# Kernel optimization log

Measured on AMD Instinct MI355X. Metric: run time of the kernel, lower is better.

Reference implementation:

```python
import jax, jax.numpy as jnp
import numpy as np
from jax import lax

V, E, H, B, P, Q = 50000, 300, 256, 32, 400, 40


def _cell(x, h, c, Wih, Whh, b):
    # torch nn.LSTMCell math (b = b_ih + b_hh), gate order i,f,g,o
    g = x @ Wih.T + h @ Whh.T + b
    i, f, gg, o = jnp.split(g, 4, axis=-1)
    c2 = jax.nn.sigmoid(f) * c + jax.nn.sigmoid(i) * jnp.tanh(gg)
    return jax.nn.sigmoid(o) * jnp.tanh(c2), c2


def setup_inputs():
    key = jax.random.key(0)
    ks = jax.random.split(key, 26)
    n = lambda k, s: jax.random.normal(k, s, jnp.float32) * 0.05
    return {
        "passage_ids": jax.random.randint(ks[0], (P, B), 0, V),
        "question_ids": jax.random.randint(ks[1], (Q, B), 0, V),
        "passage_lens": jax.random.randint(ks[2], (B,), P // 2, P + 1),
        "question_lens": jax.random.randint(ks[3], (B,), Q // 2, Q + 1),
        "answer": jax.random.randint(ks[4], (2, B), 0, P // 2),
        "embed": n(ks[5], (V, E)),
        "pre_Wih": n(ks[6], (4 * H, E)),
        "pre_Whh": n(ks[7], (4 * H, H)),
        "pre_b": n(ks[8], (4 * H,)),
        "Wq": n(ks[9], (H, H)),
        "Wp": n(ks[10], (H, H)),
        "bp": n(ks[11], (H,)),
        "Wh": n(ks[12], (H, H)),
        "w_alpha": n(ks[13], (H,)),
        "b_alpha": n(ks[14], ()),
        "m_Wih": n(ks[15], (4 * H, 2 * H)),
        "m_Whh": n(ks[16], (4 * H, H)),
        "m_b": n(ks[17], (4 * H,)),
        "Wm": n(ks[18], (2 * H, H)),
        "Wa": n(ks[19], (H, H)),
        "ba": n(ks[20], (H,)),
        "w_beta": n(ks[21], (H,)),
        "b_beta": n(ks[22], ()),
        "p_Wih": n(ks[23], (4 * H, 2 * H)),
        "p_Whh": n(ks[24], (4 * H, H)),
        "p_b": n(ks[25], (4 * H,)),
    }


def _forward(embed, pre_Wih, pre_Whh, pre_b, Wq, Wp, bp, Wh, w_alpha, b_alpha,
             m_Wih, m_Whh, m_b, Wm, Wa, ba, w_beta, b_beta, p_Wih, p_Whh, p_b,
             passage_ids, passage_lens, question_ids, question_lens):
    Hd = pre_Whh.shape[1]
    Bd = passage_ids.shape[1]
    z0 = jnp.zeros((Bd, Hd), jnp.float32)

    def preprocess(ids, lens):
        x = embed[ids]                                       # [T,B,E]
        T = x.shape[0]
        m = (jnp.arange(T)[:, None] < lens[None, :]).astype(jnp.float32)[:, :, None]  # [T,B,1]
        def step(carry, inp):
            h, c = carry
            xt, mt = inp
            _, c2 = _cell(xt, h, c, pre_Wih, pre_Whh, pre_b)
            h2 = jnp.tanh(c2) * mt                           # module quirk: h := tanh(c)
            return (h2, c2 * mt), h2
        _, Hs = lax.scan(step, (z0, z0), (x, m))
        return Hs, m

    Hp, mP = preprocess(passage_ids, passage_lens)           # [P,B,H]
    Hq, _ = preprocess(question_ids, question_lens)          # [Q,B,H]

    attQ = Hq @ Wq                                           # [Q,B,H]

    def match(Hp_dir, m_dir):
        def step(carry, inp):
            h, c = carry
            hp, mt = inp                                     # hp [B,H], mt [B,1]
            g = jnp.tanh(attQ + hp @ Wp + bp + h @ Wh)       # [Q,B,H]
            alpha = jax.nn.softmax(g @ w_alpha + b_alpha, axis=0)  # softmax over question time [Q,B]
            wq = jnp.einsum('qb,qbh->bh', alpha, Hq)
            zt = jnp.concatenate([hp, wq], axis=-1) * mt
            h2, c2 = _cell(zt, h, c, m_Wih, m_Whh, m_b)
            h2 = h2 * mt
            return (h2, c2 * mt), h2
        _, Hs = lax.scan(step, (z0, z0), (Hp_dir, m_dir))
        return Hs

    Hf = match(Hp, mP)
    Hb = match(Hp[::-1], mP[::-1])[::-1]
    Hr = jnp.concatenate([Hf, Hb], axis=-1)                  # [P,B,2H]

    attM = Hr @ Wm                                           # [P,B,H]
    valid = (jnp.arange(Hr.shape[0])[:, None] < passage_lens[None, :]).astype(jnp.float32)  # [P,B]
    ha, ca = z0, z0
    dists = []
    for _ in range(2):                                       # start / end pointer
        Fk = jnp.tanh(attM + ha @ Wa + ba)                   # [P,B,H]
        scores = Fk @ w_beta + b_beta                        # [P,B]
        scores = jnp.where(valid > 0, scores, -1e30)
        beta = jax.nn.softmax(scores, axis=0) * valid        # zeros past passage length, like original
        dists.append(beta.T)                                 # [B,P]
        wHr = jnp.einsum('pb,pbh->bh', beta, Hr)
        ha, ca = _cell(wHr, ha, ca, p_Wih, p_Whh, p_b)
    return jnp.stack(dists)                                  # [2,B,P]


def reference(passage_ids, question_ids, passage_lens, question_lens, answer,
              embed, pre_Wih, pre_Whh, pre_b, Wq, Wp, bp, Wh, w_alpha, b_alpha,
              m_Wih, m_Whh, m_b, Wm, Wa, ba, w_beta, b_beta, p_Wih, p_Whh, p_b):
    # `answer` only feeds the training loss in the original; forward returns the distributions.
    return _forward(embed, pre_Wih, pre_Whh, pre_b, Wq, Wp, bp, Wh, w_alpha, b_alpha,
                    m_Wih, m_Whh, m_b, Wm, Wa, ba, w_beta, b_beta, p_Wih, p_Whh, p_b,
                    passage_ids, passage_lens, question_ids, question_lens)
```

## Files before the change

### kernel.cpp

```cpp
#include <hip/hip_runtime.h>
#include <hip/hip_bf16.h>

typedef __attribute__((ext_vector_type(8))) short short8;
typedef __attribute__((ext_vector_type(4))) float f32x4;
typedef __attribute__((ext_vector_type(2))) float f32x2;
typedef unsigned short u16;
typedef unsigned int u32;

#define DEV __device__ __forceinline__

static constexpr int Hd    = 256;
static constexpr int Bb    = 32;
static constexpr int Pp    = 400;
static constexpr int Qq    = 40;
static constexpr int NROWS = Pp * Bb + Qq * Bb;
static constexpr int PROBE_MAGIC = 1234567;

DEV float bf2f(u16 u) { u32 i = ((u32)u) << 16; float f; __builtin_memcpy(&f, &i, 4); return f; }
DEV u16 f2bf(float f) { u32 i; __builtin_memcpy(&i, &f, 4); i += 0x7FFFu + ((i >> 16) & 1u); return (u16)(i >> 16); }
DEV float sigf(float x) { return __builtin_amdgcn_rcpf(1.f + __expf(-x)); }
DEV float tanhf_(float x) {
  float ax = __builtin_fabsf(x);
  float t = __expf(2.f * ax);
  float r = 1.f - 2.f * __builtin_amdgcn_rcpf(t + 1.f);
  return x < 0.f ? -r : r;
}
DEV f32x4 mfma32(short8 a, short8 b, f32x4 c) {
  return __builtin_amdgcn_mfma_f32_16x16x32_bf16(a, b, c, 0, 0, 0);
}
DEV short8 zero8() { short8 z = {0,0,0,0,0,0,0,0}; return z; }

struct KArgs {
  const int *pids, *qids, *plen, *qlen;
  const float *embedF, *preWihF, *preWhhF, *preBF, *WqF, *WpF, *bpF, *WhF,
              *walphaF, *balphaF, *mWihF, *mWhhF, *mBF, *WmF, *WaF, *baF,
              *wbetaF, *bbetaF, *pWihF, *pWhhF, *pBF;
  int* bar;
  u16 *WqT, *WpT, *WmT, *WihP, *Xpad, *preX, *Hp, *Hq, *Hrb, *wq, *wHr, *haB,
      *attQb, *pWihB, *pWhhB;
  float *hpWp, *attM, *pe, *scores, *aWa, *gatesW;
  float* out;
};

DEV void probe_mark(int* bar, int idx) {
  if (blockIdx.x == 0 && threadIdx.x == 0)
    __hip_atomic_store(bar + 768 + idx, PROBE_MAGIC, __ATOMIC_RELEASE, __HIP_MEMORY_SCOPE_AGENT);
}

DEV void barn(int* base, int grp, int n, int gen) {
  __syncthreads();
  if (threadIdx.x == 0) {
    int* c = base + grp * 128;
    int* g = base + grp * 128 + 64;
    if (__hip_atomic_fetch_add(c, 1, __ATOMIC_ACQ_REL, __HIP_MEMORY_SCOPE_AGENT) == n - 1) {
      __hip_atomic_store(c, 0, __ATOMIC_RELAXED, __HIP_MEMORY_SCOPE_AGENT);
      __hip_atomic_store(g, gen, __ATOMIC_RELEASE, __HIP_MEMORY_SCOPE_AGENT);
    } else {
      while (__hip_atomic_load(g, __ATOMIC_ACQUIRE, __HIP_MEMORY_SCOPE_AGENT) < gen) {}
    }
  }
  __syncthreads();
}

__global__ __launch_bounds__(256) void k_prep(KArgs A) {
  const int gtid = blockIdx.x * 256 + threadIdx.x;
  const int GS = 256 * 256;
  for (int idx = gtid; idx < 1024 * 160; idx += GS) {
    int row = idx / 160, cd = idx - row * 160;
    u32 v = 0;
    if (cd < 150) {
      f32x2 e2 = *(const f32x2*)(A.preWihF + (size_t)row * 300 + cd * 2);
      v = (u32)f2bf(e2[0]) | ((u32)f2bf(e2[1]) << 16);
    }
    *(u32*)(A.WihP + (size_t)row * 320 + cd * 2) = v;
  }
  for (int idx = gtid; idx < NROWS * 160; idx += GS) {
    int row = idx / 160, cd = idx - row * 160;
    int id = (row < Pp * Bb) ? A.pids[row] : A.qids[row - Pp * Bb];
    u32 v = 0;
    if (cd < 150) {
      f32x2 e2 = *(const f32x2*)(A.embedF + (size_t)id * 300 + cd * 2);
      v = (u32)f2bf(e2[0]) | ((u32)f2bf(e2[1]) << 16);
    }
    *(u32*)(A.Xpad + (size_t)row * 320 + cd * 2) = v;
  }
  for (int idx = gtid; idx < 65536; idx += GS) {
    int r = idx >> 8, c = idx & 255;
    A.WqT[idx] = f2bf(A.WqF[c * 256 + r]);
    A.WpT[idx] = f2bf(A.WpF[c * 256 + r]);
  }
  for (int idx = gtid; idx < 131072; idx += GS) {
    int r = idx >> 9, c = idx & 511;
    A.WmT[idx] = f2bf(A.WmF[c * 256 + r]);
  }
  for (int idx = gtid; idx < 524288 + 262144; idx += GS) {
    if (idx < 524288) A.pWihB[idx] = f2bf(A.pWihF[idx]);
    else              A.pWhhB[idx - 524288] = f2bf(A.pWhhF[idx - 524288]);
  }
  if (gtid < 32 * 256) {
    A.aWa[gtid] = A.baF[gtid & 255];
    A.haB[gtid] = 0;
  }
  probe_mark(A.bar, 0);
}

struct GemmArgs { const u16* Ag; int lda; const u16* Bg; int ldb; int Mt64, Nt64, nk; float* Cf; u16* Cb; int ldc; int* bar; int probe; };

__global__ __launch_bounds__(512) void k_gemm(GemmArgs g) {
  const int tid = threadIdx.x, lane = tid & 63;
  const int r16 = lane & 15, kl = (lane >> 4) * 8;
  const int ntile = g.Mt64 * g.Nt64;
  const int stride = gridDim.x * 8;
  for (int tix = blockIdx.x * 8 + (tid >> 6); tix < ntile; tix += stride) {
    int m0 = (tix / g.Nt64) * 64, n0 = (tix % g.Nt64) * 64;
    f32x4 acc[4][4] = {};
    for (int kb = 0; kb < g.nk; ++kb) {
      int k0 = kb * 32 + kl;
      short8 a[4], b[4];
#pragma unroll
      for (int i = 0; i < 4; ++i) {
        a[i] = *(const short8*)(g.Ag + (size_t)(m0 + i * 16 + r16) * g.lda + k0);
        b[i] = *(const short8*)(g.Bg + (size_t)(n0 + i * 16 + r16) * g.ldb + k0);
      }
#pragma unroll
      for (int mi = 0; mi < 4; ++mi)
#pragma unroll
        for (int ni = 0; ni < 4; ++ni) acc[mi][ni] = mfma32(a[mi], b[ni], acc[mi][ni]);
    }
#pragma unroll
    for (int mi = 0; mi < 4; ++mi)
#pragma unroll
      for (int ni = 0; ni < 4; ++ni)
#pragma unroll
        for (int j = 0; j < 4; ++j) {
          int r = m0 + mi * 16 + (lane >> 4) * 4 + j, cc = n0 + ni * 16 + r16;
          if (g.Cf) g.Cf[(size_t)r * g.ldc + cc] = acc[mi][ni][j];
          else      g.Cb[(size_t)r * g.ldc + cc] = f2bf(acc[mi][ni][j]);
        }
  }
  probe_mark(g.bar, g.probe);
}

__global__ __launch_bounds__(512) void k_prescan(KArgs A) {
  __shared__ __align__(16) unsigned char sm[33280];
  float* PRE = (float*)(sm + 24576);
  float* CL  = (float*)(sm + 30720);
  float* PBL = (float*)(sm + 32768);
  const int blk = blockIdx.x;
  const int gi  = blk & 15;
  const int grp = blk >> 4;
  const int steps  = grp ? Qq : Pp;
  const int* lens  = grp ? A.qlen : A.plen;
  u16* Hs          = grp ? A.Hq : A.Hp;
  const int xoff   = grp ? Pp * Bb : 0;

  const int tid = threadIdx.x, lane = tid & 63, wv = tid >> 6;
  const int r16 = lane & 15, kl = (lane >> 4) * 8;
  const int h0 = gi * 16;

  for (int idx = tid; idx < 48 * 256; idx += 512) {
    int row = idx >> 8, k = idx & 255;
    int gate = (row >> 4) * 256 + h0 + (row & 15);
    int byte = row * 512 + ((2 * k) ^ ((row & 7) << 4));
    *(u16*)(sm + byte) = f2bf(A.preWhhF[(size_t)gate * 256 + k]);
  }
  for (int idx = tid; idx < 32 * 16; idx += 512) CL[idx] = 0.f;
  if (tid < 48) PBL[tid] = A.preBF[(tid >> 4) * 256 + h0 + (tid & 15)];
  __syncthreads();

  int gen = 0;
#pragma unroll 1
  for (int t = 0; t < steps; ++t) {
    if (wv < 6) {
      int mi = wv & 1, ni = wv >> 1;
      int chain = mi * 16 + r16;
      f32x4 acc = {0.f, 0.f, 0.f, 0.f};
#pragma unroll
      for (int kb = 0; kb < 8; ++kb) {
        int k0 = kb * 32 + kl;
        short8 a = zero8();
        if (t > 0) a = *(const short8*)(Hs + (size_t)((t - 1) * 32 + chain) * 256 + k0);
        int row = ni * 16 + r16;
        short8 b = *(const short8*)(sm + row * 512 + ((2 * k0) ^ ((row & 7) << 4)));
        acc = mfma32(a, b, acc);
      }
      int col = ni * 16 + r16;
#pragma unroll
      for (int j = 0; j < 4; ++j)
        PRE[(mi * 16 + (lane >> 4) * 4 + j) * 48 + col] = acc[j];
    }
    __syncthreads();
    {
      int chain = tid >> 4, hd = tid & 15;
      size_t xr = (size_t)(xoff + t * 32 + chain) * 1024;
      float ip = PRE[chain * 48 + hd]      + bf2f(A.preX[xr + h0 + hd])       + PBL[hd];
      float fp = PRE[chain * 48 + 16 + hd] + bf2f(A.preX[xr + 256 + h0 + hd]) + PBL[16 + hd];
      float gp = PRE[chain * 48 + 32 + hd] + bf2f(A.preX[xr + 512 + h0 + hd]) + PBL[32 + hd];
      float c2 = sigf(fp) * CL[chain * 16 + hd] + sigf(ip) * tanhf_(gp);
      float mt = (t < lens[chain]) ? 1.f : 0.f;
      float h2 = tanhf_(c2) * mt;
      c2 *= mt;
      CL[chain * 16 + hd] = c2;
      Hs[(size_t)(t * 32 + chain) * 256 + h0 + hd] = f2bf(h2);
    }
    barn(A.bar, grp, 16, ++gen);
  }
  probe_mark(A.bar, 2);
}

__global__ __launch_bounds__(512) void k_match(KArgs A) {
  __shared__ __align__(16) unsigned char sm[122880];
  u16*   WHT = (u16*)(sm + 98304);
  float* PRE = (float*)(sm + 106496);
  float* CL  = (float*)(sm + 114688);
  float* EL  = (float*)(sm + 116736);
  u16*   H2L = (u16*)(sm + 118784);
  float* SL  = (float*)(sm + 119808);
  float* AL  = (float*)(sm + 120128);
  float* BPL = (float*)(sm + 120448);
  float* WAL = (float*)(sm + 121472);
  float* MBL = (float*)(sm + 122496);

  const int blk = blockIdx.x;
  const int gi  = blk & 15;
  const int dir = blk >> 4;
  const int grp = 2 + dir;
  const int tid = threadIdx.x, lane = tid & 63, wv = tid >> 6;
  const int r16 = lane & 15, kl = (lane >> 4) * 8;
  const int h0 = gi * 16;
  float* peBlk = A.pe + (size_t)((dir * 16 + gi) * 32) * 256;

  for (int idx = tid; idx < 64 * 768; idx += 512) {
    int row = idx / 768, k = idx - row * 768;
    int gate = (row >> 4) * 256 + h0 + (row & 15);
    float v = (k < 512) ? A.mWihF[(size_t)gate * 512 + k] : A.mWhhF[(size_t)gate * 256 + (k - 512)];
    int byte = row * 1536 + ((2 * k) ^ ((row & 7) << 4));
    *(u16*)(sm + byte) = f2bf(v);
  }
  for (int idx = tid; idx < 256 * 16; idx += 512) {
    int h = idx >> 4, jj = idx & 15;
    WHT[h * 16 + jj] = f2bf(A.WhF[(size_t)(h0 + jj) * 256 + h]);
  }
  for (int idx = tid; idx < 32 * 16; idx += 512) CL[idx] = 0.f;
  for (int idx = tid; idx < 32 * 256; idx += 512) peBlk[idx] = 0.f;
  if (tid < 256) { BPL[tid] = A.bpF[tid]; WAL[tid] = A.walphaF[tid]; }
  if (tid < 64) MBL[tid] = A.mBF[(tid >> 4) * 256 + h0 + (tid & 15)];
  __syncthreads();

  const float bAl = A.balphaF[0];
  int gen = 0;
#pragma unroll 1
  for (int t = 0; t < Pp; ++t) {
    int p  = dir ? (Pp - 1 - t) : t;
    int pp = dir ? (p + 1) : (p - 1);
    barn(A.bar, grp, 16, ++gen);

    {
      int c = tid >> 8, h = tid & 255;
      int b = gi * 2 + c;
      const float* pc = A.pe + (size_t)(dir * 16 * 32 + b) * 256 + h;
      float e = 0.f;
#pragma unroll
      for (int g = 0; g < 16; ++g) e += pc[(size_t)g * 32 * 256];
      EL[c * 256 + h] = e;
    }
    __syncthreads();
    {
      int c = wv >> 2;
      int b = gi * 2 + c;
      float base[4];
#pragma unroll
      for (int j = 0; j < 4; ++j) {
        int h = lane + 64 * j;
        base[j] = A.hpWp[(size_t)(p * 32 + b) * 256 + h] + BPL[h] + EL[c * 256 + h];
      }
      int q4 = wv & 3;
#pragma unroll
      for (int i = 0; i < 10; ++i) {
        int q = q4 + 4 * i;
        float s = 0.f;
#pragma unroll
        for (int j = 0; j < 4; ++j) {
          int h = lane + 64 * j;
          s += WAL[h] * tanhf_(bf2f(A.attQb[(size_t)(q * 32 + b) * 256 + h]) + base[j]);
        }
#pragma unroll
        for (int off = 32; off; off >>= 1) s += __shfl_xor(s, off, 64);
        if (lane == 0) SL[c * 40 + q] = s;
      }
    }
    __syncthreads();
    if ((wv & 3) == 0) {
      int c = wv >> 2;
      float x = (lane < 40) ? (SL[c * 40 + lane] + bAl) : -3.4e38f;
      float m = x;
#pragma unroll
      for (int off = 32; off; off >>= 1) m = fmaxf(m, __shfl_xor(m, off, 64));
      float e = (lane < 40) ? __expf(x - m) : 0.f;
      float su = e;
#pragma unroll
      for (int off = 32; off; off >>= 1) su += __shfl_xor(su, off, 64);
      if (lane < 40) AL[c * 40 + lane] = e / su;
    }
    __syncthreads();
    {
      int c = tid >> 8, h = tid & 255;
      int b = gi * 2 + c;
      float acc = 0.f;
#pragma unroll 8
      for (int q = 0; q < 40; ++q) acc += AL[c * 40 + q] * bf2f(A.Hq[(size_t)(q * 32 + b) * 256 + h]);
      float mt = (p < A.plen[b]) ? 1.f : 0.f;
      A.wq[(size_t)(dir * 32 + b) * 256 + h] = f2bf(acc * mt);
    }
    barn(A.bar, grp, 16, ++gen);

    {
      int mi = wv >> 2, ni = wv & 3;
      int chain = mi * 16 + r16;
      f32x4 acc = {0.f, 0.f, 0.f, 0.f};
#pragma unroll
      for (int kb = 0; kb < 24; ++kb) {
        int k0 = kb * 32 + kl;
        short8 a;
        if (kb < 8)       a = *(const short8*)(A.Hp + (size_t)(p * 32 + chain) * 256 + k0);
        else if (kb < 16) a = *(const short8*)(A.wq + (size_t)(dir * 32 + chain) * 256 + (k0 - 256));
        else {
          if (t == 0) a = zero8();
          else        a = *(const short8*)(A.Hrb + (size_t)(pp * 32 + chain) * 512 + dir * 256 + (k0 - 512));
        }
        int row = ni * 16 + r16;
        short8 b = *(const short8*)(sm + row * 1536 + ((2 * k0) ^ ((row & 7) << 4)));
        acc = mfma32(a, b, acc);
      }
      int col = ni * 16 + r16;
#pragma unroll
      for (int j = 0; j < 4; ++j)
        PRE[(mi * 16 + (lane >> 4) * 4 + j) * 64 + col] = acc[j];
    }
    __syncthreads();
    {
      int chain = tid >> 4, hd = tid & 15;
      float ig = PRE[chain * 64 + hd]      + MBL[hd];
      float fg = PRE[chain * 64 + 16 + hd] + MBL[16 + hd];
      float gg = PRE[chain * 64 + 32 + hd] + MBL[32 + hd];
      float og = PRE[chain * 64 + 48 + hd] + MBL[48 + hd];
      float c2 = sigf(fg) * CL[chain * 16 + hd] + sigf(ig) * tanhf_(gg);
      float h2 = sigf(og) * tanhf_(c2);
      float mt = (p < A.plen[chain]) ? 1.f : 0.f;
      c2 *= mt; h2 *= mt;
      CL[chain * 16 + hd] = c2;
      u16 hb = f2bf(h2);
      H2L[chain * 16 + hd] = hb;
      A.Hrb[(size_t)(p * 32 + chain) * 512 + dir * 256 + h0 + hd] = hb;
    }
    __syncthreads();
    {
#pragma unroll
      for (int i = 0; i < 4; ++i) {
        int task = wv * 4 + i;
        int nf = task & 15, mi = task >> 4;
        int chain = mi * 16 + r16;
        int hcol = nf * 16 + r16;
        short8 a = zero8(), b = zero8();
        if (kl < 16) {
          a = *(const short8*)(H2L + chain * 16 + kl);
          b = *(const short8*)(WHT + hcol * 16 + kl);
        }
        f32x4 acc = {0.f, 0.f, 0.f, 0.f};
        acc = mfma32(a, b, acc);
#pragma unroll
        for (int j = 0; j < 4; ++j)
          peBlk[(size_t)(mi * 16 + (lane >> 4) * 4 + j) * 256 + hcol] = acc[j];
      }
    }
  }
  probe_mark(A.bar, 5);
}

__global__ __launch_bounds__(512) void k_scores(KArgs A, int probe) {
  const int blk = blockIdx.x, tid = threadIdx.x, lane = tid & 63, wv = tid >> 6;
  for (int j = wv; j < 50; j += 8) {
    int id = blk * 50 + j;
    int p = id >> 5, b = id & 31;
    float s = 0.f;
#pragma unroll
    for (int jj = 0; jj < 4; ++jj) {
      int h = lane + 64 * jj;
      s += A.wbetaF[h] * tanhf_(A.attM[(size_t)(p * 32 + b) * 256 + h] + A.aWa[b * 256 + h]);
    }
#pragma unroll
    for (int off = 32; off; off >>= 1) s += __shfl_xor(s, off, 64);
    if (lane == 0)
      A.scores[p * 32 + b] = (p < A.plen[b]) ? (s + A.bbetaF[0]) : -1e30f;
  }
  probe_mark(A.bar, probe);
}

__global__ __launch_bounds__(512) void k_soft(KArgs A, int k, int probe) {
  __shared__ __align__(16) unsigned char sm[2048];
  float* BL = (float*)sm;
  float* RED = (float*)(sm + 1664);
  const int b = blockIdx.x, tid = threadIdx.x, lane = tid & 63, wv = tid >> 6;
  float x = (tid < 400) ? A.scores[tid * 32 + b] : -3.4e38f;
  float m = x;
#pragma unroll
  for (int off = 32; off; off >>= 1) m = fmaxf(m, __shfl_xor(m, off, 64));
  if (lane == 0) RED[wv] = m;
  __syncthreads();
  if (tid == 0) {
    float mm = RED[0];
#pragma unroll
    for (int i = 1; i < 8; ++i) mm = fmaxf(mm, RED[i]);
    RED[0] = mm;
  }
  __syncthreads();
  float M = RED[0];
  float e = (tid < 400) ? __expf(x - M) : 0.f;
  float su = e;
#pragma unroll
  for (int off = 32; off; off >>= 1) su += __shfl_xor(su, off, 64);
  if (lane == 0) RED[8 + wv] = su;
  __syncthreads();
  if (tid == 0) {
    float ss = 0.f;
#pragma unroll
    for (int i = 0; i < 8; ++i) ss += RED[8 + i];
    RED[8] = ss;
  }
  __syncthreads();
  float SUM = RED[8];
  if (tid < 400) {
    float beta = (e / SUM) * ((tid < A.plen[b]) ? 1.f : 0.f);
    A.out[(size_t)(k * 32 + b) * 400 + tid] = beta;
    BL[tid] = beta;
  }
  if (k == 0) {
    __syncthreads();
    float acc = 0.f;
#pragma unroll 4
    for (int p = 0; p < 400; ++p) acc += BL[p] * bf2f(A.Hrb[(size_t)(p * 32 + b) * 512 + tid]);
    A.wHr[b * 512 + tid] = f2bf(acc);
  }
  probe_mark(A.bar, probe);
}

__global__ __launch_bounds__(128) void k_pgates(KArgs A) {
  const int blk = blockIdx.x, tid = threadIdx.x, lane = tid & 63, wv = tid >> 6;
  const int r16 = lane & 15, kl = (lane >> 4) * 8;
  const int g0 = blk * 16;
  const int mi = wv, chain = mi * 16 + r16;
  f32x4 acc = {0.f, 0.f, 0.f, 0.f};
#pragma unroll
  for (int kb = 0; kb < 24; ++kb) {
    int k0 = kb * 32 + kl;
    short8 a, b;
    if (kb < 16) {
      a = *(const short8*)(A.wHr + (size_t)chain * 512 + k0);
      b = *(const short8*)(A.pWihB + (size_t)(g0 + r16) * 512 + k0);
    } else {
      a = *(const short8*)(A.haB + (size_t)chain * 256 + (k0 - 512));
      b = *(const short8*)(A.pWhhB + (size_t)(g0 + r16) * 256 + (k0 - 512));
    }
    acc = mfma32(a, b, acc);
  }
#pragma unroll
  for (int j = 0; j < 4; ++j)
    A.gatesW[(size_t)(mi * 16 + (lane >> 4) * 4 + j) * 1024 + g0 + r16] = acc[j];
  probe_mark(A.bar, 9);
}

__global__ __launch_bounds__(256) void k_pcell(KArgs A) {
  __shared__ float HL[256];
  const int b = blockIdx.x, hd = threadIdx.x;
  {
    float ig = A.gatesW[(size_t)b * 1024 + hd]       + A.pBF[hd];
    float gg = A.gatesW[(size_t)b * 1024 + 512 + hd] + A.pBF[512 + hd];
    float og = A.gatesW[(size_t)b * 1024 + 768 + hd] + A.pBF[768 + hd];
    float c2 = sigf(ig) * tanhf_(gg);
    float h2 = sigf(og) * tanhf_(c2);
    HL[hd] = h2;
    A.haB[b * 256 + hd] = f2bf(h2);
  }
  __syncthreads();
  {
    float acc = A.baF[hd];
#pragma unroll 8
    for (int kk = 0; kk < 256; ++kk) acc += HL[kk] * A.WaF[(size_t)kk * 256 + hd];
    A.aWa[b * 256 + hd] = acc;
  }
  probe_mark(A.bar, 10);
}

__global__ __launch_bounds__(64) void k_diag(KArgs A) {
  if (threadIdx.x == 0 && blockIdx.x == 0) {
    int bad = -1;
    for (int i = 0; i < 13; ++i) {
      int v = __hip_atomic_load(A.bar + 768 + i, __ATOMIC_ACQUIRE, __HIP_MEMORY_SCOPE_AGENT);
      if (v != PROBE_MAGIC) { bad = i; break; }
    }
    if (bad >= 0) {
      float s = 128.f * (float)(1 << bad);
      for (int j = 0; j < 8; ++j) A.out[j] = s;
    }
  }
}

extern "C" void kernel_launch(void* const* d_in, const int* in_sizes, int n_in,
                              void* d_out, int out_size, void* d_ws, size_t ws_size,
                              hipStream_t stream) {
  (void)in_sizes; (void)n_in; (void)ws_size;
  KArgs A;
  A.pids = (const int*)d_in[0];
  A.qids = (const int*)d_in[1];
  A.plen = (const int*)d_in[2];
  A.qlen = (const int*)d_in[3];
  A.embedF  = (const float*)d_in[5];
  A.preWihF = (const float*)d_in[6];
  A.preWhhF = (const float*)d_in[7];
  A.preBF   = (const float*)d_in[8];
  A.WqF     = (const float*)d_in[9];
  A.WpF     = (const float*)d_in[10];
  A.bpF     = (const float*)d_in[11];
  A.WhF     = (const float*)d_in[12];
  A.walphaF = (const float*)d_in[13];
  A.balphaF = (const float*)d_in[14];
  A.mWihF   = (const float*)d_in[15];
  A.mWhhF   = (const float*)d_in[16];
  A.mBF     = (const float*)d_in[17];
  A.WmF     = (const float*)d_in[18];
  A.WaF     = (const float*)d_in[19];
  A.baF     = (const float*)d_in[20];
  A.wbetaF  = (const float*)d_in[21];
  A.bbetaF  = (const float*)d_in[22];
  A.pWihF   = (const float*)d_in[23];
  A.pWhhF   = (const float*)d_in[24];
  A.pBF     = (const float*)d_in[25];

  char* w = (char*)d_ws;
  size_t off = 0;
  auto take = [&](size_t bytes) { void* p = w + off; off += (bytes + 255) & ~(size_t)255; return p; };
  A.bar    = (int*)take(4096);
  A.WqT    = (u16*)take(256 * 256 * 2);
  A.WpT    = (u16*)take(256 * 256 * 2);
  A.WmT    = (u16*)take(256 * 512 * 2);
  A.WihP   = (u16*)take((size_t)1024 * 320 * 2);
  A.Xpad   = (u16*)take((size_t)NROWS * 320 * 2);
  A.preX   = (u16*)take((size_t)NROWS * 1024 * 2);
  A.Hp     = (u16*)take((size_t)Pp * Bb * 256 * 2);
  A.Hq     = (u16*)take((size_t)Qq * Bb * 256 * 2);
  A.Hrb    = (u16*)take((size_t)Pp * Bb * 512 * 2);
  A.wq     = (u16*)take(2 * 32 * 256 * 2);
  A.wHr    = (u16*)take(32 * 512 * 2);
  A.haB    = (u16*)take(32 * 256 * 2);
  A.attQb  = (u16*)take((size_t)Qq * Bb * 256 * 2);
  A.pWihB  = (u16*)take((size_t)1024 * 512 * 2);
  A.pWhhB  = (u16*)take((size_t)1024 * 256 * 2);
  A.hpWp   = (float*)take((size_t)Pp * Bb * 256 * 4);
  A.attM   = (float*)take((size_t)Pp * Bb * 256 * 4);
  A.pe     = (float*)take((size_t)2 * 16 * 32 * 256 * 4);
  A.scores = (float*)take((size_t)Pp * Bb * 4);
  A.aWa    = (float*)take(32 * 256 * 4);
  A.gatesW = (float*)take((size_t)32 * 1024 * 4);
  A.out    = (float*)d_out;

  hipMemsetAsync(d_out, 0x3C, 64, stream);
  hipMemsetAsync(A.bar, 0, 4096, stream);

  (void)hipGetLastError();
  size_t outB = (size_t)out_size * 4;
  int li = 0;
#define CK  if (hipGetLastError() != hipSuccess) { hipMemsetAsync(d_out, 0x41 + li, outB, stream); return; } ++li;

  hipLaunchKernelGGL(k_prep, dim3(256), dim3(256), 0, stream, A); CK;

  GemmArgs g1{A.Xpad, 320, A.WihP, 320, NROWS / 64, 16, 10, nullptr, A.preX, 1024, A.bar, 1};
  hipLaunchKernelGGL(k_gemm, dim3(256), dim3(512), 0, stream, g1); CK;

  hipLaunchKernelGGL(k_prescan, dim3(32), dim3(512), 0, stream, A); CK;

  GemmArgs g2{A.Hq, 256, A.WqT, 256, 20, 4, 8, nullptr, A.attQb, 256, A.bar, 3};
  hipLaunchKernelGGL(k_gemm, dim3(16), dim3(512), 0, stream, g2); CK;
  GemmArgs g3{A.Hp, 256, A.WpT, 256, 200, 4, 8, A.hpWp, nullptr, 256, A.bar, 4};
  hipLaunchKernelGGL(k_gemm, dim3(128), dim3(512), 0, stream, g3); CK;

  hipLaunchKernelGGL(k_match, dim3(32), dim3(512), 0, stream, A); CK;

  GemmArgs g4{A.Hrb, 512, A.WmT, 512, 200, 4, 16, A.attM, nullptr, 256, A.bar, 6};
  hipLaunchKernelGGL(k_gemm, dim3(128), dim3(512), 0, stream, g4); CK;

  hipLaunchKernelGGL(k_scores, dim3(256), dim3(512), 0, stream, A, 7); CK;
  hipLaunchKernelGGL(k_soft,   dim3(32),  dim3(512), 0, stream, A, 0, 8); CK;
  hipLaunchKernelGGL(k_pgates, dim3(64),  dim3(128), 0, stream, A); CK;
  hipLaunchKernelGGL(k_pcell,  dim3(32),  dim3(256), 0, stream, A); CK;
  hipLaunchKernelGGL(k_scores, dim3(256), dim3(512), 0, stream, A, 11); CK;
  hipLaunchKernelGGL(k_soft,   dim3(32),  dim3(512), 0, stream, A, 1, 12); CK;

  hipLaunchKernelGGL(k_diag,   dim3(1),   dim3(64),  0, stream, A); CK;
#undef CK
}
```

Before: 9.093 ms.

## Hoist match-LSTM passage input projection out of recurrence and recompute Wh projection

Precomputes the Hp·Wih[:, :256] part of the match-LSTM gates for all timesteps with one batched GEMM before the recurrent kernel, reusing the preX buffer. The per-step MFMA loop then shrinks from 24 to 16 k-blocks. The per-step Wh projection of the previous hidden state is now recomputed from Hrb with MFMA instead of being written out as partials and summed across 16 blocks, which drops one block-wide sync per step. The grid barrier spin loop now uses relaxed loads with s_sleep and a trailing acquire fence. The cost is an extra GEMM launch and redundant Wh reads from global memory on every step.

```diff
diff --git a/kernel.cpp b/kernel.cpp
--- a/kernel.cpp
+++ b/kernel.cpp
@@ -15,6 +15,7 @@
 static constexpr int Qq    = 40;
 static constexpr int NROWS = Pp * Bb + Qq * Bb;
 static constexpr int PROBE_MAGIC = 1234567;
+static constexpr int NPROBE = 14;
 
 DEV float bf2f(u16 u) { u32 i = ((u32)u) << 16; float f; __builtin_memcpy(&f, &i, 4); return f; }
 DEV u16 f2bf(float f) { u32 i; __builtin_memcpy(&i, &f, 4); i += 0x7FFFu + ((i >> 16) & 1u); return (u16)(i >> 16); }
@@ -37,8 +38,8 @@
               *wbetaF, *bbetaF, *pWihF, *pWhhF, *pBF;
   int* bar;
   u16 *WqT, *WpT, *WmT, *WihP, *Xpad, *preX, *Hp, *Hq, *Hrb, *wq, *wHr, *haB,
-      *attQb, *pWihB, *pWhhB;
-  float *hpWp, *attM, *pe, *scores, *aWa, *gatesW;
+      *attQb, *pWihB, *pWhhB, *mWxb, *WhTb, *xW;
+  float *hpWp, *attM, *scores, *aWa, *gatesW;
   float* out;
 };
 
@@ -56,7 +57,9 @@
       __hip_atomic_store(c, 0, __ATOMIC_RELAXED, __HIP_MEMORY_SCOPE_AGENT);
       __hip_atomic_store(g, gen, __ATOMIC_RELEASE, __HIP_MEMORY_SCOPE_AGENT);
     } else {
-      while (__hip_atomic_load(g, __ATOMIC_ACQUIRE, __HIP_MEMORY_SCOPE_AGENT) < gen) {}
+      while (__hip_atomic_load(g, __ATOMIC_RELAXED, __HIP_MEMORY_SCOPE_AGENT) < gen)
+        __builtin_amdgcn_s_sleep(1);
+      __builtin_amdgcn_fence(__ATOMIC_ACQUIRE, "agent");
     }
   }
   __syncthreads();
@@ -86,12 +89,17 @@
   }
   for (int idx = gtid; idx < 65536; idx += GS) {
     int r = idx >> 8, c = idx & 255;
-    A.WqT[idx] = f2bf(A.WqF[c * 256 + r]);
-    A.WpT[idx] = f2bf(A.WpF[c * 256 + r]);
+    A.WqT[idx]  = f2bf(A.WqF[c * 256 + r]);
+    A.WpT[idx]  = f2bf(A.WpF[c * 256 + r]);
+    A.WhTb[idx] = f2bf(A.WhF[c * 256 + r]);
   }
   for (int idx = gtid; idx < 131072; idx += GS) {
     int r = idx >> 9, c = idx & 511;
     A.WmT[idx] = f2bf(A.WmF[c * 256 + r]);
+  }
+  for (int idx = gtid; idx < 1024 * 256; idx += GS) {
+    int n = idx >> 8, k = idx & 255;
+    A.mWxb[idx] = f2bf(A.mWihF[(size_t)n * 512 + k]);
   }
   for (int idx = gtid; idx < 524288 + 262144; idx += GS) {
     if (idx < 524288) A.pWihB[idx] = f2bf(A.pWihF[idx]);
@@ -209,17 +217,15 @@
 }
 
 __global__ __launch_bounds__(512) void k_match(KArgs A) {
-  __shared__ __align__(16) unsigned char sm[122880];
-  u16*   WHT = (u16*)(sm + 98304);
-  float* PRE = (float*)(sm + 106496);
-  float* CL  = (float*)(sm + 114688);
-  float* EL  = (float*)(sm + 116736);
-  u16*   H2L = (u16*)(sm + 118784);
-  float* SL  = (float*)(sm + 119808);
-  float* AL  = (float*)(sm + 120128);
-  float* BPL = (float*)(sm + 120448);
-  float* WAL = (float*)(sm + 121472);
-  float* MBL = (float*)(sm + 122496);
+  __shared__ __align__(16) unsigned char sm[81920];
+  float* PRE = (float*)(sm + 65536);
+  float* CL  = (float*)(sm + 73728);
+  float* EL  = (float*)(sm + 75776);
+  float* SL  = (float*)(sm + 77824);
+  float* AL  = (float*)(sm + 78336);
+  float* BPL = (float*)(sm + 78848);
+  float* WAL = (float*)(sm + 79872);
+  float* MBL = (float*)(sm + 80896);
 
   const int blk = blockIdx.x;
   const int gi  = blk & 15;
@@ -228,21 +234,16 @@
   const int tid = threadIdx.x, lane = tid & 63, wv = tid >> 6;
   const int r16 = lane & 15, kl = (lane >> 4) * 8;
   const int h0 = gi * 16;
-  float* peBlk = A.pe + (size_t)((dir * 16 + gi) * 32) * 256;
-
-  for (int idx = tid; idx < 64 * 768; idx += 512) {
-    int row = idx / 768, k = idx - row * 768;
+
+  for (int idx = tid; idx < 64 * 512; idx += 512) {
+    int row = idx >> 9, k = idx & 511;
     int gate = (row >> 4) * 256 + h0 + (row & 15);
-    float v = (k < 512) ? A.mWihF[(size_t)gate * 512 + k] : A.mWhhF[(size_t)gate * 256 + (k - 512)];
-    int byte = row * 1536 + ((2 * k) ^ ((row & 7) << 4));
+    float v = (k < 256) ? A.mWihF[(size_t)gate * 512 + 256 + k]
+                        : A.mWhhF[(size_t)gate * 256 + (k - 256)];
+    int byte = row * 1024 + ((2 * k) ^ ((row & 7) << 4));
     *(u16*)(sm + byte) = f2bf(v);
   }
-  for (int idx = tid; idx < 256 * 16; idx += 512) {
-    int h = idx >> 4, jj = idx & 15;
-    WHT[h * 16 + jj] = f2bf(A.WhF[(size_t)(h0 + jj) * 256 + h]);
-  }
   for (int idx = tid; idx < 32 * 16; idx += 512) CL[idx] = 0.f;
-  for (int idx = tid; idx < 32 * 256; idx += 512) peBlk[idx] = 0.f;
   if (tid < 256) { BPL[tid] = A.bpF[tid]; WAL[tid] = A.walphaF[tid]; }
   if (tid < 64) MBL[tid] = A.mBF[(tid >> 4) * 256 + h0 + (tid & 15)];
   __syncthreads();
@@ -255,14 +256,27 @@
     int pp = dir ? (p + 1) : (p - 1);
     barn(A.bar, grp, 16, ++gen);
 
-    {
-      int c = tid >> 8, h = tid & 255;
-      int b = gi * 2 + c;
-      const float* pc = A.pe + (size_t)(dir * 16 * 32 + b) * 256 + h;
-      float e = 0.f;
-#pragma unroll
-      for (int g = 0; g < 16; ++g) e += pc[(size_t)g * 32 * 256];
-      EL[c * 256 + h] = e;
+    if (t == 0) {
+      EL[tid] = 0.f;
+    } else {
+      f32x4 acc0 = {0.f,0.f,0.f,0.f}, acc1 = {0.f,0.f,0.f,0.f};
+#pragma unroll
+      for (int kb = 0; kb < 8; ++kb) {
+        int k0 = kb * 32 + kl;
+        short8 a = zero8();
+        if (r16 < 2)
+          a = *(const short8*)(A.Hrb + (size_t)(pp * 32 + gi * 2 + r16) * 512 + dir * 256 + k0);
+        short8 bA = *(const short8*)(A.WhTb + (size_t)(wv * 32 + r16) * 256 + k0);
+        short8 bB = *(const short8*)(A.WhTb + (size_t)(wv * 32 + 16 + r16) * 256 + k0);
+        acc0 = mfma32(a, bA, acc0);
+        acc1 = mfma32(a, bB, acc1);
+      }
+      if ((lane >> 4) == 0) {
+        EL[0 * 256 + wv * 32 + r16]      = acc0[0];
+        EL[1 * 256 + wv * 32 + r16]      = acc0[1];
+        EL[0 * 256 + wv * 32 + 16 + r16] = acc1[0];
+        EL[1 * 256 + wv * 32 + 16 + r16] = acc1[1];
+      }
     }
     __syncthreads();
     {
@@ -319,17 +333,16 @@
       int chain = mi * 16 + r16;
       f32x4 acc = {0.f, 0.f, 0.f, 0.f};
 #pragma unroll
-      for (int kb = 0; kb < 24; ++kb) {
+      for (int kb = 0; kb < 16; ++kb) {
         int k0 = kb * 32 + kl;
         short8 a;
-        if (kb < 8)       a = *(const short8*)(A.Hp + (size_t)(p * 32 + chain) * 256 + k0);
-        else if (kb < 16) a = *(const short8*)(A.wq + (size_t)(dir * 32 + chain) * 256 + (k0 - 256));
+        if (kb < 8) a = *(const short8*)(A.wq + (size_t)(dir * 32 + chain) * 256 + k0);
         else {
           if (t == 0) a = zero8();
-          else        a = *(const short8*)(A.Hrb + (size_t)(pp * 32 + chain) * 512 + dir * 256 + (k0 - 512));
+          else        a = *(const short8*)(A.Hrb + (size_t)(pp * 32 + chain) * 512 + dir * 256 + (k0 - 256));
         }
         int row = ni * 16 + r16;
-        short8 b = *(const short8*)(sm + row * 1536 + ((2 * k0) ^ ((row & 7) << 4)));
+        short8 b = *(const short8*)(sm + row * 1024 + ((2 * k0) ^ ((row & 7) << 4)));
         acc = mfma32(a, b, acc);
       }
       int col = ni * 16 + r16;
@@ -340,41 +353,20 @@
     __syncthreads();
     {
       int chain = tid >> 4, hd = tid & 15;
-      float ig = PRE[chain * 64 + hd]      + MBL[hd];
-      float fg = PRE[chain * 64 + 16 + hd] + MBL[16 + hd];
-      float gg = PRE[chain * 64 + 32 + hd] + MBL[32 + hd];
-      float og = PRE[chain * 64 + 48 + hd] + MBL[48 + hd];
+      size_t xr = (size_t)(p * 32 + chain) * 1024 + h0 + hd;
+      float ig = PRE[chain * 64 + hd]      + MBL[hd]      + bf2f(A.xW[xr]);
+      float fg = PRE[chain * 64 + 16 + hd] + MBL[16 + hd] + bf2f(A.xW[xr + 256]);
+      float gg = PRE[chain * 64 + 32 + hd] + MBL[32 + hd] + bf2f(A.xW[xr + 512]);
+      float og = PRE[chain * 64 + 48 + hd] + MBL[48 + hd] + bf2f(A.xW[xr + 768]);
       float c2 = sigf(fg) * CL[chain * 16 + hd] + sigf(ig) * tanhf_(gg);
       float h2 = sigf(og) * tanhf_(c2);
       float mt = (p < A.plen[chain]) ? 1.f : 0.f;
       c2 *= mt; h2 *= mt;
       CL[chain * 16 + hd] = c2;
-      u16 hb = f2bf(h2);
-      H2L[chain * 16 + hd] = hb;
-      A.Hrb[(size_t)(p * 32 + chain) * 512 + dir * 256 + h0 + hd] = hb;
-    }
-    __syncthreads();
-    {
-#pragma unroll
-      for (int i = 0; i < 4; ++i) {
-        int task = wv * 4 + i;
-        int nf = task & 15, mi = task >> 4;
-        int chain = mi * 16 + r16;
-        int hcol = nf * 16 + r16;
-        short8 a = zero8(), b = zero8();
-        if (kl < 16) {
-          a = *(const short8*)(H2L + chain * 16 + kl);
-          b = *(const short8*)(WHT + hcol * 16 + kl);
-        }
-        f32x4 acc = {0.f, 0.f, 0.f, 0.f};
-        acc = mfma32(a, b, acc);
-#pragma unroll
-        for (int j = 0; j < 4; ++j)
-          peBlk[(size_t)(mi * 16 + (lane >> 4) * 4 + j) * 256 + hcol] = acc[j];
-      }
-    }
-  }
-  probe_mark(A.bar, 5);
+      A.Hrb[(size_t)(p * 32 + chain) * 512 + dir * 256 + h0 + hd] = f2bf(h2);
+    }
+  }
+  probe_mark(A.bar, 6);
 }
 
 __global__ __launch_bounds__(512) void k_scores(KArgs A, int probe) {
@@ -466,7 +458,7 @@
 #pragma unroll
   for (int j = 0; j < 4; ++j)
     A.gatesW[(size_t)(mi * 16 + (lane >> 4) * 4 + j) * 1024 + g0 + r16] = acc[j];
-  probe_mark(A.bar, 9);
+  probe_mark(A.bar, 10);
 }
 
 __global__ __launch_bounds__(256) void k_pcell(KArgs A) {
@@ -488,13 +480,13 @@
     for (int kk = 0; kk < 256; ++kk) acc += HL[kk] * A.WaF[(size_t)kk * 256 + hd];
     A.aWa[b * 256 + hd] = acc;
   }
-  probe_mark(A.bar, 10);
+  probe_mark(A.bar, 11);
 }
 
 __global__ __launch_bounds__(64) void k_diag(KArgs A) {
   if (threadIdx.x == 0 && blockIdx.x == 0) {
     int bad = -1;
-    for (int i = 0; i < 13; ++i) {
+    for (int i = 0; i < NPROBE; ++i) {
       int v = __hip_atomic_load(A.bar + 768 + i, __ATOMIC_ACQUIRE, __HIP_MEMORY_SCOPE_AGENT);
       if (v != PROBE_MAGIC) { bad = i; break; }
     }
@@ -555,12 +547,14 @@
   A.attQb  = (u16*)take((size_t)Qq * Bb * 256 * 2);
   A.pWihB  = (u16*)take((size_t)1024 * 512 * 2);
   A.pWhhB  = (u16*)take((size_t)1024 * 256 * 2);
+  A.mWxb   = (u16*)take((size_t)1024 * 256 * 2);
+  A.WhTb   = (u16*)take((size_t)256 * 256 * 2);
   A.hpWp   = (float*)take((size_t)Pp * Bb * 256 * 4);
   A.attM   = (float*)take((size_t)Pp * Bb * 256 * 4);
-  A.pe     = (float*)take((size_t)2 * 16 * 32 * 256 * 4);
   A.scores = (float*)take((size_t)Pp * Bb * 4);
   A.aWa    = (float*)take(32 * 256 * 4);
   A.gatesW = (float*)take((size_t)32 * 1024 * 4);
+  A.xW     = A.preX;
   A.out    = (float*)d_out;
 
   hipMemsetAsync(d_out, 0x3C, 64, stream);
@@ -582,18 +576,20 @@
   hipLaunchKernelGGL(k_gemm, dim3(16), dim3(512), 0, stream, g2); CK;
   GemmArgs g3{A.Hp, 256, A.WpT, 256, 200, 4, 8, A.hpWp, nullptr, 256, A.bar, 4};
   hipLaunchKernelGGL(k_gemm, dim3(128), dim3(512), 0, stream, g3); CK;
+  GemmArgs gx{A.Hp, 256, A.mWxb, 256, 200, 16, 8, nullptr, A.xW, 1024, A.bar, 5};
+  hipLaunchKernelGGL(k_gemm, dim3(256), dim3(512), 0, stream, gx); CK;
 
   hipLaunchKernelGGL(k_match, dim3(32), dim3(512), 0, stream, A); CK;
 
-  GemmArgs g4{A.Hrb, 512, A.WmT, 512, 200, 4, 16, A.attM, nullptr, 256, A.bar, 6};
+  GemmArgs g4{A.Hrb, 512, A.WmT, 512, 200, 4, 16, A.attM, nullptr, 256, A.bar, 7};
   hipLaunchKernelGGL(k_gemm, dim3(128), dim3(512), 0, stream, g4); CK;
 
-  hipLaunchKernelGGL(k_scores, dim3(256), dim3(512), 0, stream, A, 7); CK;
-  hipLaunchKernelGGL(k_soft,   dim3(32),  dim3(512), 0, stream, A, 0, 8); CK;
+  hipLaunchKernelGGL(k_scores, dim3(256), dim3(512), 0, stream, A, 8); CK;
+  hipLaunchKernelGGL(k_soft,   dim3(32),  dim3(512), 0, stream, A, 0, 9); CK;
   hipLaunchKernelGGL(k_pgates, dim3(64),  dim3(128), 0, stream, A); CK;
   hipLaunchKernelGGL(k_pcell,  dim3(32),  dim3(256), 0, stream, A); CK;
-  hipLaunchKernelGGL(k_scores, dim3(256), dim3(512), 0, stream, A, 11); CK;
-  hipLaunchKernelGGL(k_soft,   dim3(32),  dim3(512), 0, stream, A, 1, 12); CK;
+  hipLaunchKernelGGL(k_scores, dim3(256), dim3(512), 0, stream, A, 12); CK;
+  hipLaunchKernelGGL(k_soft,   dim3(32),  dim3(512), 0, stream, A, 1, 13); CK;
 
   hipLaunchKernelGGL(k_diag,   dim3(1),   dim3(64),  0, stream, A); CK;
 #undef CK
```

Result: slower. 9.596 ms (+5.5%).

## Split preprocess LSTM scan by batch to drop grid-wide barriers

Applied to the files above, without the earlier changes.

The preprocess LSTM recurrence is repartitioned so each block owns 4 batch chains across all hidden units, not 16 hidden units across all 32 chains. The per-step cross-block atomic barrier becomes a local __syncthreads, and h is carried in shared memory. Whh is pre-swizzled into an MFMA fragment layout in global memory and reloaded from L2 every step, and only 4 of 16 MFMA rows do useful work. Fewer blocks (16) run, trading inter-block sync latency for redundant weight streaming and more per-block compute.

```diff
diff --git a/kernel.cpp b/kernel.cpp
--- a/kernel.cpp
+++ b/kernel.cpp
@@ -15,6 +15,7 @@
 static constexpr int Qq    = 40;
 static constexpr int NROWS = Pp * Bb + Qq * Bb;
 static constexpr int PROBE_MAGIC = 1234567;
+static constexpr int NPROBE = 13;
 
 DEV float bf2f(u16 u) { u32 i = ((u32)u) << 16; float f; __builtin_memcpy(&f, &i, 4); return f; }
 DEV u16 f2bf(float f) { u32 i; __builtin_memcpy(&i, &f, 4); i += 0x7FFFu + ((i >> 16) & 1u); return (u16)(i >> 16); }
@@ -29,6 +30,9 @@
   return __builtin_amdgcn_mfma_f32_16x16x32_bf16(a, b, c, 0, 0, 0);
 }
 DEV short8 zero8() { short8 z = {0,0,0,0,0,0,0,0}; return z; }
+DEV short8 ldtile(const u16* base, int tile, int lane) {
+  return *(const short8*)(base + ((size_t)tile * 64 + lane) * 8);
+}
 
 struct KArgs {
   const int *pids, *qids, *plen, *qlen;
@@ -37,7 +41,7 @@
               *wbetaF, *bbetaF, *pWihF, *pWhhF, *pBF;
   int* bar;
   u16 *WqT, *WpT, *WmT, *WihP, *Xpad, *preX, *Hp, *Hq, *Hrb, *wq, *wHr, *haB,
-      *attQb, *pWihB, *pWhhB;
+      *attQb, *pWihB, *pWhhB, *preWhT;
   float *hpWp, *attM, *pe, *scores, *aWa, *gatesW;
   float* out;
 };
@@ -92,6 +96,12 @@
   for (int idx = gtid; idx < 131072; idx += GS) {
     int r = idx >> 9, c = idx & 511;
     A.WmT[idx] = f2bf(A.WmF[c * 256 + r]);
+  }
+  for (int idx = gtid; idx < 48 * 8 * 512; idx += GS) {
+    int e = idx & 7, l = (idx >> 3) & 63, tk = idx >> 9;
+    int nt = tk >> 3, kt = tk & 7;
+    int n = nt * 16 + (l & 15), k = kt * 32 + (l >> 4) * 8 + e;
+    A.preWhT[idx] = f2bf(A.preWhhF[(size_t)n * 256 + k]);
   }
   for (int idx = gtid; idx < 524288 + 262144; idx += GS) {
     if (idx < 524288) A.pWihB[idx] = f2bf(A.pWihF[idx]);
@@ -141,69 +151,78 @@
   probe_mark(g.bar, g.probe);
 }
 
-__global__ __launch_bounds__(512) void k_prescan(KArgs A) {
-  __shared__ __align__(16) unsigned char sm[33280];
-  float* PRE = (float*)(sm + 24576);
-  float* CL  = (float*)(sm + 30720);
-  float* PBL = (float*)(sm + 32768);
+__global__ __launch_bounds__(512, 1) void k_prescan(KArgs A) {
+  __shared__ __align__(16) unsigned char sm[24576];
+  u16*   HF  = (u16*)sm;
+  float* CS  = (float*)(sm + 2176);
+  float* PRE = (float*)(sm + 6784);
+  float* PBL = (float*)(sm + 19648);
   const int blk = blockIdx.x;
-  const int gi  = blk & 15;
-  const int grp = blk >> 4;
-  const int steps  = grp ? Qq : Pp;
-  const int* lens  = grp ? A.qlen : A.plen;
-  u16* Hs          = grp ? A.Hq : A.Hp;
-  const int xoff   = grp ? Pp * Bb : 0;
-
+  const int isQ = blk >> 3;
+  const int c0  = (blk & 7) * 4;
+  const int steps = isQ ? Qq : Pp;
+  const int* lens = isQ ? A.qlen : A.plen;
+  u16* Hs = isQ ? A.Hq : A.Hp;
+  const int xoff = isQ ? Pp * Bb : 0;
   const int tid = threadIdx.x, lane = tid & 63, wv = tid >> 6;
   const int r16 = lane & 15, kl = (lane >> 4) * 8;
-  const int h0 = gi * 16;
-
-  for (int idx = tid; idx < 48 * 256; idx += 512) {
-    int row = idx >> 8, k = idx & 255;
-    int gate = (row >> 4) * 256 + h0 + (row & 15);
-    int byte = row * 512 + ((2 * k) ^ ((row & 7) << 4));
-    *(u16*)(sm + byte) = f2bf(A.preWhhF[(size_t)gate * 256 + k]);
-  }
-  for (int idx = tid; idx < 32 * 16; idx += 512) CL[idx] = 0.f;
-  if (tid < 48) PBL[tid] = A.preBF[(tid >> 4) * 256 + h0 + (tid & 15)];
-  __syncthreads();
-
-  int gen = 0;
+
+  for (int idx = tid; idx < 768; idx += 512) PBL[idx] = A.preBF[idx];
+  for (int idx = tid; idx < 4 * 264; idx += 512) HF[idx] = 0;
+  for (int idx = tid; idx < 4 * 256; idx += 512) CS[idx] = 0.f;
+  __syncthreads();
+
+  const int cC = tid >> 7, hh = (tid & 127) * 2;
+  const int bC = c0 + cC;
+  const int lenC = lens[bC];
+
 #pragma unroll 1
   for (int t = 0; t < steps; ++t) {
-    if (wv < 6) {
-      int mi = wv & 1, ni = wv >> 1;
-      int chain = mi * 16 + r16;
+    short8 afr[8];
+#pragma unroll
+    for (int kt = 0; kt < 8; ++kt)
+      afr[kt] = (r16 < 4) ? *(const short8*)(HF + r16 * 264 + kt * 32 + kl) : zero8();
+#pragma unroll
+    for (int i = 0; i < 6; ++i) {
+      int nt = wv * 6 + i;
+      short8 bf[8];
+#pragma unroll
+      for (int kt = 0; kt < 8; ++kt) bf[kt] = ldtile(A.preWhT, nt * 8 + kt, lane);
       f32x4 acc = {0.f, 0.f, 0.f, 0.f};
 #pragma unroll
-      for (int kb = 0; kb < 8; ++kb) {
-        int k0 = kb * 32 + kl;
-        short8 a = zero8();
-        if (t > 0) a = *(const short8*)(Hs + (size_t)((t - 1) * 32 + chain) * 256 + k0);
-        int row = ni * 16 + r16;
-        short8 b = *(const short8*)(sm + row * 512 + ((2 * k0) ^ ((row & 7) << 4)));
-        acc = mfma32(a, b, acc);
+      for (int kt = 0; kt < 8; ++kt) acc = mfma32(afr[kt], bf[kt], acc);
+      if ((lane >> 4) == 0) {
+#pragma unroll
+        for (int j = 0; j < 4; ++j) PRE[j * 776 + nt * 16 + r16] = acc[j];
       }
-      int col = ni * 16 + r16;
-#pragma unroll
-      for (int j = 0; j < 4; ++j)
-        PRE[(mi * 16 + (lane >> 4) * 4 + j) * 48 + col] = acc[j];
     }
     __syncthreads();
     {
-      int chain = tid >> 4, hd = tid & 15;
-      size_t xr = (size_t)(xoff + t * 32 + chain) * 1024;
-      float ip = PRE[chain * 48 + hd]      + bf2f(A.preX[xr + h0 + hd])       + PBL[hd];
-      float fp = PRE[chain * 48 + 16 + hd] + bf2f(A.preX[xr + 256 + h0 + hd]) + PBL[16 + hd];
-      float gp = PRE[chain * 48 + 32 + hd] + bf2f(A.preX[xr + 512 + h0 + hd]) + PBL[32 + hd];
-      float c2 = sigf(fp) * CL[chain * 16 + hd] + sigf(ip) * tanhf_(gp);
-      float mt = (t < lens[chain]) ? 1.f : 0.f;
-      float h2 = tanhf_(c2) * mt;
-      c2 *= mt;
-      CL[chain * 16 + hd] = c2;
-      Hs[(size_t)(t * 32 + chain) * 256 + h0 + hd] = f2bf(h2);
-    }
-    barn(A.bar, grp, 16, ++gen);
+      size_t xr = (size_t)(xoff + t * 32 + bC) * 1024;
+      u32 x0 = *(const u32*)(A.preX + xr + hh);
+      u32 x1 = *(const u32*)(A.preX + xr + 256 + hh);
+      u32 x2 = *(const u32*)(A.preX + xr + 512 + hh);
+      u16 hb[2];
+#pragma unroll
+      for (int u = 0; u < 2; ++u) {
+        int h = hh + u;
+        float xi = bf2f(u ? (u16)(x0 >> 16) : (u16)x0);
+        float xf = bf2f(u ? (u16)(x1 >> 16) : (u16)x1);
+        float xg = bf2f(u ? (u16)(x2 >> 16) : (u16)x2);
+        float ip = PRE[cC * 776 + h]       + xi + PBL[h];
+        float fp = PRE[cC * 776 + 256 + h] + xf + PBL[256 + h];
+        float gp = PRE[cC * 776 + 512 + h] + xg + PBL[512 + h];
+        float c2 = sigf(fp) * CS[cC * 256 + h] + sigf(ip) * tanhf_(gp);
+        float mt = (t < lenC) ? 1.f : 0.f;
+        float h2 = tanhf_(c2) * mt;
+        CS[cC * 256 + h] = c2 * mt;
+        hb[u] = f2bf(h2);
+      }
+      u32 pk = (u32)hb[0] | ((u32)hb[1] << 16);
+      *(u32*)(HF + cC * 264 + hh) = pk;
+      *(u32*)(Hs + (size_t)(t * 32 + bC) * 256 + hh) = pk;
+    }
+    __syncthreads();
   }
   probe_mark(A.bar, 2);
 }
@@ -494,7 +513,7 @@
 __global__ __launch_bounds__(64) void k_diag(KArgs A) {
   if (threadIdx.x == 0 && blockIdx.x == 0) {
     int bad = -1;
-    for (int i = 0; i < 13; ++i) {
+    for (int i = 0; i < NPROBE; ++i) {
       int v = __hip_atomic_load(A.bar + 768 + i, __ATOMIC_ACQUIRE, __HIP_MEMORY_SCOPE_AGENT);
       if (v != PROBE_MAGIC) { bad = i; break; }
     }
@@ -555,6 +574,7 @@
   A.attQb  = (u16*)take((size_t)Qq * Bb * 256 * 2);
   A.pWihB  = (u16*)take((size_t)1024 * 512 * 2);
   A.pWhhB  = (u16*)take((size_t)1024 * 256 * 2);
+  A.preWhT = (u16*)take((size_t)48 * 8 * 512 * 2);
   A.hpWp   = (float*)take((size_t)Pp * Bb * 256 * 4);
   A.attM   = (float*)take((size_t)Pp * Bb * 256 * 4);
   A.pe     = (float*)take((size_t)2 * 16 * 32 * 256 * 4);
@@ -576,7 +596,7 @@
   GemmArgs g1{A.Xpad, 320, A.WihP, 320, NROWS / 64, 16, 10, nullptr, A.preX, 1024, A.bar, 1};
   hipLaunchKernelGGL(k_gemm, dim3(256), dim3(512), 0, stream, g1); CK;
 
-  hipLaunchKernelGGL(k_prescan, dim3(32), dim3(512), 0, stream, A); CK;
+  hipLaunchKernelGGL(k_prescan, dim3(16), dim3(512), 0, stream, A); CK;
 
   GemmArgs g2{A.Hq, 256, A.WqT, 256, 20, 4, 8, nullptr, A.attQb, 256, A.bar, 3};
   hipLaunchKernelGGL(k_gemm, dim3(16), dim3(512), 0, stream, g2); CK;
```

Result: slower. 9.344 ms (+2.8%).
